# Optimization experiments

Measured on AMD Instinct MI355X. Metric: run time of the kernel, lower is better.

Reference implementation:

```python
import jax, jax.numpy as jnp
import numpy as np

K, D, N, T, B = 8, 16, 32, 200, 2048
_LOG2PI = float(np.log(2.0 * np.pi))


def setup_inputs() -> dict:
    key = jax.random.key(0)
    ks = jax.random.split(key, 13)
    return {
        "discrete_states": jax.random.randint(ks[0], (B, T), 0, K),
        "continuous_states": jax.random.normal(ks[1], (B, T, D), dtype=jnp.float32),
        "obs": jax.random.normal(ks[2], (B, T, N), dtype=jnp.float32),
        "discrete_init_logits": jax.random.normal(ks[3], (K,), dtype=jnp.float32),
        "continuous_init_locs": jax.random.normal(ks[4], (K, D), dtype=jnp.float32),
        "continuous_init_log_scales": jax.random.normal(ks[5], (K, D), dtype=jnp.float32),
        "state_transition_logits": jax.random.normal(ks[6], (K, K), dtype=jnp.float32),
        "dynamics_matrices": jax.random.normal(ks[7], (K, D, D), dtype=jnp.float32) * 0.3,
        "dynamics_offsets": jax.random.normal(ks[8], (K, D), dtype=jnp.float32),
        # NOTE: original code uses dynamics_log_scales directly as a scale (missing .exp());
        # we keep that math faithfully but init it strictly positive to stay finite.
        "dynamics_log_scales": jax.random.uniform(ks[9], (K, D), minval=0.5, maxval=1.5, dtype=jnp.float32),
        "emission_matrices": jax.random.normal(ks[10], (K, N, D), dtype=jnp.float32),
        "emission_offsets": jax.random.normal(ks[11], (K, N), dtype=jnp.float32),
        "emission_log_scales": jax.random.normal(ks[12], (K, N), dtype=jnp.float32),
    }


def _normal_lp(x, loc, scale):
    # elementwise Normal log-prob
    return -0.5 * jnp.square((x - loc) / scale) - jnp.log(scale) - 0.5 * _LOG2PI


def reference(discrete_states, continuous_states, obs,
              discrete_init_logits, continuous_init_locs, continuous_init_log_scales,
              state_transition_logits, dynamics_matrices, dynamics_offsets,
              dynamics_log_scales, emission_matrices, emission_offsets,
              emission_log_scales):
    """log p(s_{1:T}, z_{1:T}, x_{1:T}) -> [B]"""
    s0 = discrete_states[:, 0]                      # [B]
    z0 = continuous_states[:, 0]                    # [B,D]
    # p(s_1)
    lp = jax.nn.log_softmax(discrete_init_logits)[s0]
    # p(z_1 | s_1)
    lp = lp + _normal_lp(z0, continuous_init_locs[s0],
                         jnp.exp(continuous_init_log_scales[s0])).sum(-1)
    # p(s_t | s_{t-1}) for t=2..T, fully vectorized over time
    s_prev = discrete_states[:, :-1]
    s_cur = discrete_states[:, 1:]
    trans = jax.nn.log_softmax(state_transition_logits, axis=-1)  # [K,K]
    lp = lp + trans[s_prev, s_cur].sum(-1)
    # p(z_t | z_{t-1}, s_t)
    A = dynamics_matrices[s_cur]                    # [B,T-1,D,D] gather
    dyn_loc = jnp.einsum('btij,btj->bti', A, continuous_states[:, :-1]) + dynamics_offsets[s_cur]
    dyn_scale = dynamics_log_scales[s_cur]          # faithful: original omits .exp()
    lp = lp + _normal_lp(continuous_states[:, 1:], dyn_loc, dyn_scale).sum((-1, -2))
    # p(x_t | z_t, s_t) for all t
    C = emission_matrices[discrete_states]          # [B,T,N,D] gather
    em_loc = jnp.einsum('btij,btj->bti', C, continuous_states) + emission_offsets[discrete_states]
    em_scale = jnp.exp(emission_log_scales[discrete_states])
    lp = lp + _normal_lp(obs, em_loc, em_scale).sum((-1, -2))
    return lp
```

## Files before the change

### kernel.cpp

```cpp
#include <hip/hip_runtime.h>

#define KK 8
#define DD 16
#define NN 32
#define TT 200
#define BB 2048

#define SC 516
#define SA 260
#define SE 36
#define SD 20

__device__ __forceinline__ float dot16(const float* __restrict__ row,
                                       const float* __restrict__ z) {
  const float4* r4 = reinterpret_cast<const float4*>(row);
  float4 c0 = r4[0], c1 = r4[1], c2 = r4[2], c3 = r4[3];
  float a = c0.x * z[0], b = c0.y * z[1];
  a = fmaf(c0.z, z[2], a);  b = fmaf(c0.w, z[3], b);
  a = fmaf(c1.x, z[4], a);  b = fmaf(c1.y, z[5], b);
  a = fmaf(c1.z, z[6], a);  b = fmaf(c1.w, z[7], b);
  a = fmaf(c2.x, z[8], a);  b = fmaf(c2.y, z[9], b);
  a = fmaf(c2.z, z[10], a); b = fmaf(c2.w, z[11], b);
  a = fmaf(c3.x, z[12], a); b = fmaf(c3.y, z[13], b);
  a = fmaf(c3.z, z[14], a); b = fmaf(c3.w, z[15], b);
  return a + b;
}

__device__ __forceinline__ void load16(float* __restrict__ d,
                                       const float* __restrict__ s) {
  const float4* p = reinterpret_cast<const float4*>(s);
  float4 a0 = p[0], a1 = p[1], a2 = p[2], a3 = p[3];
  d[0] = a0.x;  d[1] = a0.y;  d[2] = a0.z;  d[3] = a0.w;
  d[4] = a1.x;  d[5] = a1.y;  d[6] = a1.z;  d[7] = a1.w;
  d[8] = a2.x;  d[9] = a2.y;  d[10] = a2.z; d[11] = a2.w;
  d[12] = a3.x; d[13] = a3.y; d[14] = a3.z; d[15] = a3.w;
}

__global__ __launch_bounds__(512) void slds_lp_kernel(
    const int* __restrict__ dsts,
    const float* __restrict__ zg,
    const float* __restrict__ obsg,
    const float* __restrict__ initlg,
    const float* __restrict__ initloc,
    const float* __restrict__ initls,
    const float* __restrict__ transg,
    const float* __restrict__ Ag,
    const float* __restrict__ dynoff,
    const float* __restrict__ dynls,
    const float* __restrict__ Cg,
    const float* __restrict__ emoff,
    const float* __restrict__ emls,
    float* __restrict__ out)
{
  __shared__ __align__(16) float sC[KK * SC];
  __shared__ __align__(16) float sA[KK * SA];
  __shared__ __align__(16) float sEmOff[KK * SE];
  __shared__ __align__(16) float sEmInv[KK * SE];
  __shared__ __align__(16) float sDynOff[KK * SD];
  __shared__ __align__(16) float sDynInv[KK * SD];
  __shared__ float sTrans[KK * KK];
  __shared__ float sEmConst[KK];
  __shared__ float sDynConst[KK];
  __shared__ float sInitLp[KK];

  const float HALF_LOG2PI = 0.91893853320467274178f;
  const int tid = threadIdx.x;

  for (int i = tid; i < KK * NN * DD; i += 512) {
    int k = i >> 9, r = i & 511;
    sC[k * SC + r] = Cg[i];
  }
  for (int i = tid; i < KK * DD * DD; i += 512) {
    int k = i >> 8, r = i & 255;
    sA[k * SA + r] = Ag[i];
  }
  if (tid < KK * NN) {
    int k = tid >> 5, n = tid & 31;
    sEmOff[k * SE + n] = emoff[tid];
    sEmInv[k * SE + n] = expf(-emls[tid]);
  }
  if (tid < KK * DD) {
    int k = tid >> 4, d = tid & 15;
    sDynOff[k * SD + d] = dynoff[tid];
    sDynInv[k * SD + d] = 1.0f / dynls[tid];
  }
  if (tid < KK * KK) {
    int kr = tid >> 3;
    float mx = transg[kr * KK];
    for (int j = 1; j < KK; ++j) mx = fmaxf(mx, transg[kr * KK + j]);
    float ss = 0.f;
    for (int j = 0; j < KK; ++j) ss += expf(transg[kr * KK + j] - mx);
    sTrans[tid] = transg[tid] - (logf(ss) + mx);
  }
  if (tid < KK) {
    int k = tid;
    float se = 0.f;
    for (int n = 0; n < NN; ++n) se -= emls[k * NN + n];
    sEmConst[k] = se - NN * HALF_LOG2PI;
    float sd = 0.f;
    for (int d = 0; d < DD; ++d) sd -= logf(dynls[k * DD + d]);
    sDynConst[k] = sd - DD * HALF_LOG2PI;
    float mx = initlg[0];
    for (int j = 1; j < KK; ++j) mx = fmaxf(mx, initlg[j]);
    float ss = 0.f;
    for (int j = 0; j < KK; ++j) ss += expf(initlg[j] - mx);
    float si = 0.f;
    for (int d = 0; d < DD; ++d) si -= initls[k * DD + d];
    sInitLp[k] = initlg[k] - (logf(ss) + mx) + si - DD * HALF_LOG2PI;
  }
  __syncthreads();

  if (tid < 400) {
    const int item = blockIdx.x * 400 + tid;
    const int b = item / TT;
    const int t = item - b * TT;

    float z[16];
    load16(z, zg + (size_t)item * DD);
    const int s = dsts[item];
    float lp;

    if (t != 0) {
      const int sp = dsts[item - 1];
      float zp[16];
      load16(zp, zg + (size_t)(item - 1) * DD);
      const float* __restrict__ Ab = &sA[s * SA];
      const int db4 = s * (SD / 4);
      float a2acc = 0.f;
#pragma unroll
      for (int g = 0; g < 4; ++g) {
        const int i0 = g * 4;
        float4 off = reinterpret_cast<const float4*>(sDynOff)[db4 + g];
        float4 inv = reinterpret_cast<const float4*>(sDynInv)[db4 + g];
        float l0 = dot16(&Ab[(i0 + 0) * DD], zp) + off.x;
        float l1 = dot16(&Ab[(i0 + 1) * DD], zp) + off.y;
        float l2 = dot16(&Ab[(i0 + 2) * DD], zp) + off.z;
        float l3 = dot16(&Ab[(i0 + 3) * DD], zp) + off.w;
        float d0 = (z[i0 + 0] - l0) * inv.x;
        float d1 = (z[i0 + 1] - l1) * inv.y;
        float d2 = (z[i0 + 2] - l2) * inv.z;
        float d3 = (z[i0 + 3] - l3) * inv.w;
        a2acc = fmaf(d0, d0, a2acc); a2acc = fmaf(d1, d1, a2acc);
        a2acc = fmaf(d2, d2, a2acc); a2acc = fmaf(d3, d3, a2acc);
      }
      lp = -0.5f * a2acc + sDynConst[s] + sTrans[sp * KK + s];
    } else {
      const float* __restrict__ ploc = initloc + s * DD;
      const float* __restrict__ pls  = initls + s * DD;
      float a2acc = 0.f;
#pragma unroll
      for (int g = 0; g < 4; ++g) {
        const int i0 = g * 4;
        float4 loc = reinterpret_cast<const float4*>(ploc)[g];
        float4 ls  = reinterpret_cast<const float4*>(pls)[g];
        float d0 = (z[i0 + 0] - loc.x) * expf(-ls.x);
        float d1 = (z[i0 + 1] - loc.y) * expf(-ls.y);
        float d2 = (z[i0 + 2] - loc.z) * expf(-ls.z);
        float d3 = (z[i0 + 3] - loc.w) * expf(-ls.w);
        a2acc = fmaf(d0, d0, a2acc); a2acc = fmaf(d1, d1, a2acc);
        a2acc = fmaf(d2, d2, a2acc); a2acc = fmaf(d3, d3, a2acc);
      }
      lp = -0.5f * a2acc + sInitLp[s];
    }

    {
      const float4* o4 = reinterpret_cast<const float4*>(obsg + (size_t)item * NN);
      const int cb = s * SC;
      const int eb4 = s * (SE / 4);
      float acc = 0.f;
#pragma unroll 1
      for (int g = 0; g < 8; ++g) {
        float4 o = o4[g];
        float4 off = reinterpret_cast<const float4*>(sEmOff)[eb4 + g];
        float4 inv = reinterpret_cast<const float4*>(sEmInv)[eb4 + g];
        int n0 = g * 4;
        float l0 = dot16(&sC[cb + (n0 + 0) * DD], z) + off.x;
        float l1 = dot16(&sC[cb + (n0 + 1) * DD], z) + off.y;
        float l2 = dot16(&sC[cb + (n0 + 2) * DD], z) + off.z;
        float l3 = dot16(&sC[cb + (n0 + 3) * DD], z) + off.w;
        float d0 = (o.x - l0) * inv.x;
        float d1 = (o.y - l1) * inv.y;
        float d2 = (o.z - l2) * inv.z;
        float d3 = (o.w - l3) * inv.w;
        acc = fmaf(d0, d0, acc); acc = fmaf(d1, d1, acc);
        acc = fmaf(d2, d2, acc); acc = fmaf(d3, d3, acc);
      }
      lp += -0.5f * acc + sEmConst[s];
    }

    const int lane = tid & 63;
    float v = lp;
#pragma unroll
    for (int off = 1; off < 64; off <<= 1) {
      float ov = __shfl_up(v, off, 64);
      int obk = __shfl_up(b, off, 64);
      if (lane >= off && obk == b) v += ov;
    }
    int nb = __shfl_down(b, 1, 64);
    if (lane == 63 || tid == 399 || nb != b) atomicAdd(&out[b], v);
  }
}

extern "C" void kernel_launch(void* const* d_in, const int* in_sizes, int n_in,
                              void* d_out, int out_size, void* d_ws, size_t ws_size,
                              hipStream_t stream) {
  const int*   dsts    = (const int*)d_in[0];
  const float* zg      = (const float*)d_in[1];
  const float* obsg    = (const float*)d_in[2];
  const float* initlg  = (const float*)d_in[3];
  const float* initloc = (const float*)d_in[4];
  const float* initls  = (const float*)d_in[5];
  const float* transg  = (const float*)d_in[6];
  const float* Ag      = (const float*)d_in[7];
  const float* dynoff  = (const float*)d_in[8];
  const float* dynls   = (const float*)d_in[9];
  const float* Cg      = (const float*)d_in[10];
  const float* emoff   = (const float*)d_in[11];
  const float* emls    = (const float*)d_in[12];
  float* out = (float*)d_out;

  hipMemsetAsync(d_out, 0, BB * sizeof(float), stream);

  slds_lp_kernel<<<1024, 512, 0, stream>>>(dsts, zg, obsg, initlg, initloc,
                                           initls, transg, Ag, dynoff, dynls,
                                           Cg, emoff, emls, out);
}
```

Before: 139.4 us.

## Sort items by discrete state so each wavefront uses one uniform matrix

Adds a histogram, scan and scatter pipeline that buckets (b,t) items by discrete state, padding each bucket to a multiple of 64. The main kernel then reads a wave-uniform state, so the A and C matrices are fetched from global memory with scalar or broadcast loads rather than copied into LDS by every block. Per-item log-probs go to a workspace array, and a separate reduction kernel sums them per batch. This removes divergent LDS gathers and the per-block staging of large shared arrays. In exchange it adds four extra launches, a single-block scan, a large memset, and scattered, non-coalesced reads of z and obs.

Measured after the change: 184.7 us. 1.32x slower.

```diff
diff --git a/kernel.cpp b/kernel.cpp
--- a/kernel.cpp
+++ b/kernel.cpp
@@ -5,6 +5,19 @@
 #define NN 32
 #define TT 200
 #define BB 2048
+#define NITEMS (BB * TT)
+#define NBLK_H 1024
+#define CHUNK (NITEMS / NBLK_H)
+#define SLOTS 410112
+#define NBLK_MAIN (SLOTS / 256)
+
+#define WS_HIST_OFF 0
+#define WS_HIST_BYTES (NBLK_H * KK * 4)
+#define WS_SIDX_OFF (WS_HIST_OFF + WS_HIST_BYTES)
+#define WS_SIDX_BYTES (SLOTS * 4)
+#define WS_LP_OFF (WS_SIDX_OFF + WS_SIDX_BYTES)
+#define WS_LP_BYTES (NITEMS * 4)
+#define WS_NEEDED ((size_t)(WS_LP_OFF + WS_LP_BYTES))
 
 #define SC 516
 #define SA 260
@@ -36,7 +49,81 @@
   d[12] = a3.x; d[13] = a3.y; d[14] = a3.z; d[15] = a3.w;
 }
 
-__global__ __launch_bounds__(512) void slds_lp_kernel(
+__global__ __launch_bounds__(256) void hist_kernel(const int* __restrict__ dsts,
+                                                   int* __restrict__ hist) {
+  __shared__ int h[KK];
+  const int tid = threadIdx.x;
+  if (tid < KK) h[tid] = 0;
+  __syncthreads();
+  const int base = blockIdx.x * CHUNK;
+  for (int ofs = tid; ofs < CHUNK; ofs += 256)
+    atomicAdd(&h[dsts[base + ofs]], 1);
+  __syncthreads();
+  if (tid < KK) hist[blockIdx.x * KK + tid] = h[tid];
+}
+
+__global__ __launch_bounds__(256) void scan_kernel(int* __restrict__ hist) {
+  __shared__ int ht[KK * NBLK_H];
+  __shared__ int partial[KK * 32];
+  __shared__ int cnt[KK];
+  __shared__ int bbase[KK];
+  const int tid = threadIdx.x;
+  for (int i = tid; i < KK * NBLK_H; i += 256) {
+    int blk = i >> 3, k = i & 7;
+    ht[k * NBLK_H + blk] = hist[i];
+  }
+  __syncthreads();
+  const int k = tid >> 5, j = tid & 31;
+  {
+    int s = 0;
+    for (int q = 0; q < 32; ++q) s += ht[k * NBLK_H + j * 32 + q];
+    partial[k * 32 + j] = s;
+  }
+  __syncthreads();
+  if (tid < KK) {
+    int run = 0;
+    for (int j2 = 0; j2 < 32; ++j2) {
+      int v = partial[tid * 32 + j2];
+      partial[tid * 32 + j2] = run;
+      run += v;
+    }
+    cnt[tid] = run;
+  }
+  __syncthreads();
+  if (tid == 0) {
+    int cur = 0;
+    for (int kk2 = 0; kk2 < KK; ++kk2) {
+      bbase[kk2] = cur;
+      cur = (cur + cnt[kk2] + 63) & ~63;
+    }
+  }
+  __syncthreads();
+  int run = bbase[k] + partial[k * 32 + j];
+  for (int q = 0; q < 32; ++q) {
+    int blk = j * 32 + q;
+    int v = ht[k * NBLK_H + blk];
+    hist[blk * KK + k] = run;
+    run += v;
+  }
+}
+
+__global__ __launch_bounds__(256) void scatter_kernel(const int* __restrict__ dsts,
+                                                      const int* __restrict__ hist,
+                                                      int* __restrict__ sidx) {
+  __shared__ int cur[KK];
+  const int tid = threadIdx.x;
+  if (tid < KK) cur[tid] = hist[blockIdx.x * KK + tid];
+  __syncthreads();
+  const int base = blockIdx.x * CHUNK;
+  for (int ofs = tid; ofs < CHUNK; ofs += 256) {
+    int item = base + ofs;
+    int pos = atomicAdd(&cur[dsts[item]], 1);
+    sidx[pos] = item;
+  }
+}
+
+__global__ __launch_bounds__(256) void slds_lp_main(
+    const int* __restrict__ sidx,
     const int* __restrict__ dsts,
     const float* __restrict__ zg,
     const float* __restrict__ obsg,
@@ -50,10 +137,8 @@
     const float* __restrict__ Cg,
     const float* __restrict__ emoff,
     const float* __restrict__ emls,
-    float* __restrict__ out)
+    float* __restrict__ lpArr)
 {
-  __shared__ __align__(16) float sC[KK * SC];
-  __shared__ __align__(16) float sA[KK * SA];
   __shared__ __align__(16) float sEmOff[KK * SE];
   __shared__ __align__(16) float sEmInv[KK * SE];
   __shared__ __align__(16) float sDynOff[KK * SD];
@@ -66,14 +151,6 @@
   const float HALF_LOG2PI = 0.91893853320467274178f;
   const int tid = threadIdx.x;
 
-  for (int i = tid; i < KK * NN * DD; i += 512) {
-    int k = i >> 9, r = i & 511;
-    sC[k * SC + r] = Cg[i];
-  }
-  for (int i = tid; i < KK * DD * DD; i += 512) {
-    int k = i >> 8, r = i & 255;
-    sA[k * SA + r] = Ag[i];
-  }
   if (tid < KK * NN) {
     int k = tid >> 5, n = tid & 31;
     sEmOff[k * SE + n] = emoff[tid];
@@ -110,16 +187,180 @@
   }
   __syncthreads();
 
+  const int slot = blockIdx.x * 256 + tid;
+  int idx = sidx[slot];
+  const int idx0 = __builtin_amdgcn_readfirstlane(idx);
+  if (idx0 < 0) return;
+  const bool valid = idx >= 0;
+  const int idxc = valid ? idx : idx0;
+  const int su = __builtin_amdgcn_readfirstlane(dsts[idx0]);
+
+  const int t = idxc - (idxc / TT) * TT;
+
+  float z[16];
+  load16(z, zg + (size_t)idxc * DD);
+  float lp;
+
+  if (t != 0) {
+    const int sp = dsts[idxc - 1];
+    float zp[16];
+    load16(zp, zg + (size_t)(idxc - 1) * DD);
+    const float* __restrict__ Ab = Ag + (size_t)su * (DD * DD);
+    const int db4 = su * (SD / 4);
+    float a2acc = 0.f;
+#pragma unroll
+    for (int g = 0; g < 4; ++g) {
+      const int i0 = g * 4;
+      float4 off = reinterpret_cast<const float4*>(sDynOff)[db4 + g];
+      float4 inv = reinterpret_cast<const float4*>(sDynInv)[db4 + g];
+      float l0 = dot16(&Ab[(i0 + 0) * DD], zp) + off.x;
+      float l1 = dot16(&Ab[(i0 + 1) * DD], zp) + off.y;
+      float l2 = dot16(&Ab[(i0 + 2) * DD], zp) + off.z;
+      float l3 = dot16(&Ab[(i0 + 3) * DD], zp) + off.w;
+      float d0 = (z[i0 + 0] - l0) * inv.x;
+      float d1 = (z[i0 + 1] - l1) * inv.y;
+      float d2 = (z[i0 + 2] - l2) * inv.z;
+      float d3 = (z[i0 + 3] - l3) * inv.w;
+      a2acc = fmaf(d0, d0, a2acc); a2acc = fmaf(d1, d1, a2acc);
+      a2acc = fmaf(d2, d2, a2acc); a2acc = fmaf(d3, d3, a2acc);
+    }
+    lp = -0.5f * a2acc + sDynConst[su] + sTrans[sp * KK + su];
+  } else {
+    const float* __restrict__ ploc = initloc + su * DD;
+    const float* __restrict__ pls  = initls + su * DD;
+    float a2acc = 0.f;
+#pragma unroll
+    for (int g = 0; g < 4; ++g) {
+      const int i0 = g * 4;
+      float4 loc = reinterpret_cast<const float4*>(ploc)[g];
+      float4 ls  = reinterpret_cast<const float4*>(pls)[g];
+      float d0 = (z[i0 + 0] - loc.x) * expf(-ls.x);
+      float d1 = (z[i0 + 1] - loc.y) * expf(-ls.y);
+      float d2 = (z[i0 + 2] - loc.z) * expf(-ls.z);
+      float d3 = (z[i0 + 3] - loc.w) * expf(-ls.w);
+      a2acc = fmaf(d0, d0, a2acc); a2acc = fmaf(d1, d1, a2acc);
+      a2acc = fmaf(d2, d2, a2acc); a2acc = fmaf(d3, d3, a2acc);
+    }
+    lp = -0.5f * a2acc + sInitLp[su];
+  }
+
+  {
+    const float* __restrict__ Cs = Cg + (size_t)su * (NN * DD);
+    const float4* o4 = reinterpret_cast<const float4*>(obsg + (size_t)idxc * NN);
+    const int eb4 = su * (SE / 4);
+    float acc = 0.f;
+#pragma unroll 1
+    for (int g = 0; g < 8; ++g) {
+      float4 o = o4[g];
+      float4 off = reinterpret_cast<const float4*>(sEmOff)[eb4 + g];
+      float4 inv = reinterpret_cast<const float4*>(sEmInv)[eb4 + g];
+      int n0 = g * 4;
+      float l0 = dot16(&Cs[(n0 + 0) * DD], z) + off.x;
+      float l1 = dot16(&Cs[(n0 + 1) * DD], z) + off.y;
+      float l2 = dot16(&Cs[(n0 + 2) * DD], z) + off.z;
+      float l3 = dot16(&Cs[(n0 + 3) * DD], z) + off.w;
+      float d0 = (o.x - l0) * inv.x;
+      float d1 = (o.y - l1) * inv.y;
+      float d2 = (o.z - l2) * inv.z;
+      float d3 = (o.w - l3) * inv.w;
+      acc = fmaf(d0, d0, acc); acc = fmaf(d1, d1, acc);
+      acc = fmaf(d2, d2, acc); acc = fmaf(d3, d3, acc);
+    }
+    lp += -0.5f * acc + sEmConst[su];
+  }
+
+  if (valid) lpArr[idx] = lp;
+}
+
+__global__ __launch_bounds__(256) void reduce_kernel(const float* __restrict__ lpArr,
+                                                     float* __restrict__ out) {
+  const int tid = threadIdx.x;
+  const int item = blockIdx.x * 256 + tid;
+  const int b = item / TT;
+  float v = lpArr[item];
+  const int lane = tid & 63;
+#pragma unroll
+  for (int off = 1; off < 64; off <<= 1) {
+    float ov = __shfl_up(v, off, 64);
+    int obk = __shfl_up(b, off, 64);
+    if (lane >= off && obk == b) v += ov;
+  }
+  int nb = __shfl_down(b, 1, 64);
+  if (lane == 63 || nb != b) atomicAdd(&out[b], v);
+}
+
+__global__ __launch_bounds__(512) void slds_lp_kernel(
+    const int* __restrict__ dsts, const float* __restrict__ zg,
+    const float* __restrict__ obsg, const float* __restrict__ initlg,
+    const float* __restrict__ initloc, const float* __restrict__ initls,
+    const float* __restrict__ transg, const float* __restrict__ Ag,
+    const float* __restrict__ dynoff, const float* __restrict__ dynls,
+    const float* __restrict__ Cg, const float* __restrict__ emoff,
+    const float* __restrict__ emls, float* __restrict__ out)
+{
+  __shared__ __align__(16) float sC[KK * SC];
+  __shared__ __align__(16) float sA[KK * SA];
+  __shared__ __align__(16) float sEmOff[KK * SE];
+  __shared__ __align__(16) float sEmInv[KK * SE];
+  __shared__ __align__(16) float sDynOff[KK * SD];
+  __shared__ __align__(16) float sDynInv[KK * SD];
+  __shared__ float sTrans[KK * KK];
+  __shared__ float sEmConst[KK];
+  __shared__ float sDynConst[KK];
+  __shared__ float sInitLp[KK];
+  const float HALF_LOG2PI = 0.91893853320467274178f;
+  const int tid = threadIdx.x;
+  for (int i = tid; i < KK * NN * DD; i += 512) {
+    int k = i >> 9, r = i & 511;
+    sC[k * SC + r] = Cg[i];
+  }
+  for (int i = tid; i < KK * DD * DD; i += 512) {
+    int k = i >> 8, r = i & 255;
+    sA[k * SA + r] = Ag[i];
+  }
+  if (tid < KK * NN) {
+    int k = tid >> 5, n = tid & 31;
+    sEmOff[k * SE + n] = emoff[tid];
+    sEmInv[k * SE + n] = expf(-emls[tid]);
+  }
+  if (tid < KK * DD) {
+    int k = tid >> 4, d = tid & 15;
+    sDynOff[k * SD + d] = dynoff[tid];
+    sDynInv[k * SD + d] = 1.0f / dynls[tid];
+  }
+  if (tid < KK * KK) {
+    int kr = tid >> 3;
+    float mx = transg[kr * KK];
+    for (int j = 1; j < KK; ++j) mx = fmaxf(mx, transg[kr * KK + j]);
+    float ss = 0.f;
+    for (int j = 0; j < KK; ++j) ss += expf(transg[kr * KK + j] - mx);
+    sTrans[tid] = transg[tid] - (logf(ss) + mx);
+  }
+  if (tid < KK) {
+    int k = tid;
+    float se = 0.f;
+    for (int n = 0; n < NN; ++n) se -= emls[k * NN + n];
+    sEmConst[k] = se - NN * HALF_LOG2PI;
+    float sd = 0.f;
+    for (int d = 0; d < DD; ++d) sd -= logf(dynls[k * DD + d]);
+    sDynConst[k] = sd - DD * HALF_LOG2PI;
+    float mx = initlg[0];
+    for (int j = 1; j < KK; ++j) mx = fmaxf(mx, initlg[j]);
+    float ss = 0.f;
+    for (int j = 0; j < KK; ++j) ss += expf(initlg[j] - mx);
+    float si = 0.f;
+    for (int d = 0; d < DD; ++d) si -= initls[k * DD + d];
+    sInitLp[k] = initlg[k] - (logf(ss) + mx) + si - DD * HALF_LOG2PI;
+  }
+  __syncthreads();
   if (tid < 400) {
     const int item = blockIdx.x * 400 + tid;
     const int b = item / TT;
     const int t = item - b * TT;
-
     float z[16];
     load16(z, zg + (size_t)item * DD);
     const int s = dsts[item];
     float lp;
-
     if (t != 0) {
       const int sp = dsts[item - 1];
       float zp[16];
@@ -162,7 +403,6 @@
       }
       lp = -0.5f * a2acc + sInitLp[s];
     }
-
     {
       const float4* o4 = reinterpret_cast<const float4*>(obsg + (size_t)item * NN);
       const int cb = s * SC;
@@ -187,7 +427,6 @@
       }
       lp += -0.5f * acc + sEmConst[s];
     }
-
     const int lane = tid & 63;
     float v = lp;
 #pragma unroll
@@ -221,7 +460,25 @@
 
   hipMemsetAsync(d_out, 0, BB * sizeof(float), stream);
 
-  slds_lp_kernel<<<1024, 512, 0, stream>>>(dsts, zg, obsg, initlg, initloc,
-                                           initls, transg, Ag, dynoff, dynls,
-                                           Cg, emoff, emls, out);
-}
+  if (d_ws == nullptr || ws_size < WS_NEEDED) {
+    slds_lp_kernel<<<1024, 512, 0, stream>>>(dsts, zg, obsg, initlg, initloc,
+                                             initls, transg, Ag, dynoff, dynls,
+                                             Cg, emoff, emls, out);
+    return;
+  }
+
+  int*   hist  = (int*)((char*)d_ws + WS_HIST_OFF);
+  int*   sidx  = (int*)((char*)d_ws + WS_SIDX_OFF);
+  float* lpArr = (float*)((char*)d_ws + WS_LP_OFF);
+
+  hipMemsetAsync(sidx, 0xFF, WS_SIDX_BYTES, stream);
+
+  hist_kernel<<<NBLK_H, 256, 0, stream>>>(dsts, hist);
+  scan_kernel<<<1, 256, 0, stream>>>(hist);
+  scatter_kernel<<<NBLK_H, 256, 0, stream>>>(dsts, hist, sidx);
+  slds_lp_main<<<NBLK_MAIN, 256, 0, stream>>>(sidx, dsts, zg, obsg, initlg,
+                                              initloc, initls, transg, Ag,
+                                              dynoff, dynls, Cg, emoff, emls,
+                                              lpArr);
+  reduce_kernel<<<NITEMS / 256, 256, 0, stream>>>(lpArr, out);
+}
```
